# Kernel tuning notes

Measured on AMD Instinct MI355X. Metric: run time of the kernel, lower is better.

Reference implementation:

```python
import jax, jax.numpy as jnp
import numpy as np

IMG = 640.0  # square input image, strides 16/32 -> 40x40 and 20x20 grids

def _decode_level(raw, stride):
    # raw: [B, 5+C, H, W] -> [B, H*W, 5+C] with xy/wh decoded (get_output_and_grid)
    b, ch, h, w = raw.shape
    out = raw.transpose(0, 2, 3, 1).reshape(b, h * w, ch)
    yv, xv = jnp.meshgrid(jnp.arange(h), jnp.arange(w), indexing='ij')
    gx = xv.reshape(-1).astype(raw.dtype)
    gy = yv.reshape(-1).astype(raw.dtype)
    xy = (out[..., :2] + jnp.stack([gx, gy], -1)[None]) * stride
    wh = jnp.exp(out[..., 2:4]) * stride
    out = jnp.concatenate([xy, wh, out[..., 4:]], -1)
    return out, gx, gy, jnp.full((h * w,), stride, raw.dtype)

def _pairwise_iou(a, b):
    # a:[M,4], b:[A,4] in cxcywh -> [M,A] (bboxes_iou, xyxy=False)
    tl = jnp.maximum(a[:, None, :2] - a[:, None, 2:] * 0.5, b[None, :, :2] - b[None, :, 2:] * 0.5)
    br = jnp.minimum(a[:, None, :2] + a[:, None, 2:] * 0.5, b[None, :, :2] + b[None, :, 2:] * 0.5)
    inter = jnp.prod(br - tl, -1) * (tl < br).all(-1)
    area_a = a[:, 2] * a[:, 3]
    area_b = b[:, 2] * b[:, 3]
    return inter / (area_a[:, None] + area_b[None, :] - inter + 1e-16)

def _iou_loss(p, t):
    # YOLOX IOUloss (loss_type='iou'): 1 - iou^2, elementwise over [..., 4] cxcywh
    tl = jnp.maximum(p[..., :2] - p[..., 2:] * 0.5, t[..., :2] - t[..., 2:] * 0.5)
    br = jnp.minimum(p[..., :2] + p[..., 2:] * 0.5, t[..., :2] + t[..., 2:] * 0.5)
    inter = jnp.prod(br - tl, -1) * (tl < br).all(-1)
    iou = inter / (p[..., 2] * p[..., 3] + t[..., 2] * t[..., 3] - inter + 1e-16)
    return 1.0 - iou ** 2

def _bce_logits(x, t):
    # BCEWithLogitsLoss(reduction='none') = softplus(x) - x*t (stable)
    return jnp.logaddexp(0.0, x) - x * t

def _assign_one(bbox_p, cls_p, obj_p, gtb, gtc, gtv, ax, ay, st):
    # SimOTA assignment for one image (mask form of get_assignments, which is @no_grad).
    # bbox_p:[A,4] cls_p:[A,C] obj_p:[A] gtb:[M,4] px cxcywh, gtv:[M] valid mask.
    m = gtb.shape[0]
    axc = (ax + 0.5) * st
    ayc = (ay + 0.5) * st
    gl = gtb[:, 0] - 0.5 * gtb[:, 2]; gr = gtb[:, 0] + 0.5 * gtb[:, 2]
    gtp = gtb[:, 1] - 0.5 * gtb[:, 3]; gbt = gtb[:, 1] + 0.5 * gtb[:, 3]
    in_box = ((axc[None] > gl[:, None]) & (axc[None] < gr[:, None]) &
              (ayc[None] > gtp[:, None]) & (ayc[None] < gbt[:, None])) & gtv[:, None]
    r = 2.5  # center_radius
    in_ctr = ((axc[None] > gtb[:, 0:1] - r * st[None]) & (axc[None] < gtb[:, 0:1] + r * st[None]) &
              (ayc[None] > gtb[:, 1:2] - r * st[None]) & (ayc[None] < gtb[:, 1:2] + r * st[None])) & gtv[:, None]
    fg_cand = (in_box | in_ctr).any(0)          # candidate anchors (fg_mask pre-filter)
    in_both = in_box & in_ctr
    ious = _pairwise_iou(gtb, bbox_p)            # [M,A]
    p = jnp.sqrt(jax.nn.sigmoid(cls_p) * jax.nn.sigmoid(obj_p)[:, None])[None]  # [1,A,C]
    t = jax.nn.one_hot(gtc, cls_p.shape[-1], dtype=p.dtype)[:, None, :]          # [M,1,C]
    eps = 1e-12
    cls_cost = -(t * jnp.log(p + eps) + (1.0 - t) * jnp.log(1.0 - p + eps)).sum(-1)
    invalid = (~fg_cand)[None] | (~gtv)[:, None]
    cost = cls_cost - 3.0 * jnp.log(ious + 1e-8) + 1e5 * (~in_both) + 1e9 * invalid
    ious_m = jnp.where(invalid, 0.0, ious)
    topk, _ = jax.lax.top_k(ious_m, 10)
    dk = jnp.maximum(topk.sum(-1).astype(jnp.int32), 1)  # dynamic_k, clamp min=1
    dk = jnp.where(gtv, dk, 0)
    ranks = jnp.argsort(jnp.argsort(cost, axis=1), axis=1)
    matching = ranks < dk[:, None]                        # top dynamic_k lowest-cost anchors per gt
    conflict = matching.sum(0) > 1
    best_gt = jnp.argmin(cost, 0)
    matching = jnp.where(conflict[None], jnp.arange(m)[:, None] == best_gt[None], matching)
    fg = matching.any(0)
    matched = jnp.argmax(matching, 0).astype(jnp.int32)
    pred_iou = jnp.where(matching, ious, 0.0).sum(0)
    return fg, matched, pred_iou

def _forward(out_l0, out_l1, gt_boxes, gt_classes, num_gts):
    ncls = out_l0.shape[1] - 5
    decs, xs, ys, ss = [], [], [], []
    for raw, stride in ((out_l0, 16.0), (out_l1, 32.0)):
        d, gx, gy, s = _decode_level(raw, stride)
        decs.append(d); xs.append(gx); ys.append(gy); ss.append(s)
    outputs = jnp.concatenate(decs, 1)  # [B, A, 5+C]
    ax = jnp.concatenate(xs); ay = jnp.concatenate(ys); st = jnp.concatenate(ss)
    bbox_p = outputs[..., :4]; obj_p = outputs[..., 4]; cls_p = outputs[..., 5:]
    gtb = gt_boxes * IMG  # normalized -> pixels (imgs_w == imgs_h == IMG)
    gtv = jnp.arange(gt_boxes.shape[1])[None, :] < num_gts[:, None]
    sg = jax.lax.stop_gradient  # get_assignments runs under torch.no_grad
    fg, matched, pred_iou = jax.vmap(_assign_one, in_axes=(0, 0, 0, 0, 0, 0, None, None, None))(
        sg(bbox_p), sg(cls_p), sg(obj_p), sg(gtb), gt_classes, gtv, ax, ay, st)
    fgf = fg.astype(outputs.dtype)
    cls_t = jax.nn.one_hot(jnp.take_along_axis(gt_classes, matched, 1), ncls,
                           dtype=outputs.dtype) * pred_iou[..., None] * fgf[..., None]
    reg_t = jnp.take_along_axis(gtb, matched[..., None], 1)  # [B,A,4]
    num_fg = jnp.maximum(fgf.sum(), 1.0)
    loss_iou = (_iou_loss(bbox_p, reg_t) * fgf).sum() / num_fg
    loss_obj = _bce_logits(obj_p, fgf).sum() / num_fg
    loss_cls = (_bce_logits(cls_p, cls_t) * fgf[..., None]).sum() / num_fg
    total = 5.0 * loss_iou + loss_obj + loss_cls
    return (total, 5.0 * loss_iou, loss_obj, loss_cls,
            num_fg / jnp.maximum(num_gts.sum().astype(outputs.dtype), 1.0))

def setup_inputs() -> dict:
    key = jax.random.key(0)
    k1, k2, k3, k4, k5 = jax.random.split(key, 5)
    return {
        'out_l0': jax.random.normal(k1, (64, 25, 40, 40), jnp.float32),
        'out_l1': jax.random.normal(k2, (64, 25, 20, 20), jnp.float32),
        'gt_boxes': jax.random.uniform(k3, (64, 100, 4), jnp.float32, 1e-3, 1.0),
        'gt_classes': jax.random.randint(k4, (64, 100), 0, 20).astype(jnp.int32),
        'num_gts': jax.random.randint(k5, (64,), 0, 100).astype(jnp.int32),
    }

def reference(out_l0, out_l1, gt_boxes, gt_classes, num_gts):
    return _forward(out_l0, out_l1, gt_boxes, gt_classes, num_gts)
```

## Files before the change

kernel.cpp:

```cpp
#include <hip/hip_runtime.h>
#include <cfloat>
#include <climits>

#define NB 64
#define NA 2000
#define NAP 2048
#define NA0 1600
#define NC 20
#define NM 100

__device__ __forceinline__ void anchor_geom(int a, float& axc, float& ayc, float& st) {
    if (a < NA0) {
        st = 16.0f;
        int x = a % 40, y = a / 40;
        axc = ((float)x + 0.5f) * 16.0f;
        ayc = ((float)y + 0.5f) * 16.0f;
    } else {
        st = 32.0f;
        int aa = a - NA0;
        int x = aa % 20, y = aa / 20;
        axc = ((float)x + 0.5f) * 32.0f;
        ayc = ((float)y + 0.5f) * 32.0f;
    }
}

__device__ __forceinline__ float cost_pair(const float4 g, float clsc, const float4 pb,
                                           float axc, float ayc, float st, bool fc) {
    float tlx = fmaxf(g.x - 0.5f * g.z, pb.x - 0.5f * pb.z);
    float tly = fmaxf(g.y - 0.5f * g.w, pb.y - 0.5f * pb.w);
    float brx = fminf(g.x + 0.5f * g.z, pb.x + 0.5f * pb.z);
    float bry = fminf(g.y + 0.5f * g.w, pb.y + 0.5f * pb.w);
    float inter = (brx - tlx) * (bry - tly);
    bool ok = (tlx < brx) && (tly < bry);
    inter = ok ? inter : 0.0f;
    float iou = inter / ((g.z * g.w + pb.z * pb.w) - inter + 1e-16f);
    bool ib = (axc > g.x - 0.5f * g.z) && (axc < g.x + 0.5f * g.z)
           && (ayc > g.y - 0.5f * g.w) && (ayc < g.y + 0.5f * g.w);
    bool ic = (axc > g.x - 2.5f * st) && (axc < g.x + 2.5f * st)
           && (ayc > g.y - 2.5f * st) && (ayc < g.y + 2.5f * st);
    return ((clsc - 3.0f * __logf(iou + 1e-8f)) + ((ib && ic) ? 0.0f : 1e5f)) + (fc ? 0.0f : 1e9f);
}

__global__ __launch_bounds__(256) void k_decode(const float* __restrict__ l0, const float* __restrict__ l1,
                                                const float* __restrict__ gt_boxes, const int* __restrict__ num_gts,
                                                float4* __restrict__ dec, float* __restrict__ qq,
                                                unsigned long long* __restrict__ fgw, unsigned int* __restrict__ cm,
                                                unsigned int* __restrict__ counter) {
    int b = blockIdx.y;
    int a = blockIdx.x * 256 + threadIdx.x;
    int lane = threadIdx.x & 63;
    __shared__ float4 sext[NM];
    __shared__ float2 sctr[NM];
    __shared__ int sng;
    if (threadIdx.x < NM) {
        float4 g = ((const float4*)gt_boxes)[b * NM + threadIdx.x];
        g.x *= 640.0f; g.y *= 640.0f; g.z *= 640.0f; g.w *= 640.0f;
        sext[threadIdx.x] = make_float4(g.x - 0.5f * g.z, g.x + 0.5f * g.z,
                                        g.y - 0.5f * g.w, g.y + 0.5f * g.w);
        sctr[threadIdx.x] = make_float2(g.x, g.y);
    }
    if (threadIdx.x == 0) sng = num_gts[b];
    if (b == 0 && blockIdx.x == 0 && threadIdx.x == 0) *counter = 0u;
    __syncthreads();

    bool real = a < NA;
    size_t pidx = (size_t)b * NAP + a;

    if (!real) {
        dec[pidx] = make_float4(0.f, 0.f, 0.f, 0.f);
#pragma unroll
        for (int c = 0; c < NC; c++) qq[((size_t)b * NC + c) * NAP + a] = 0.0f;
        cm[pidx] = 0;
        unsigned long long mk = __ballot(0);
        if (lane == 0) fgw[(size_t)b * 32 + (a >> 6)] = mk;
        return;
    }

    float v[25];
    if (a < NA0) {
        const float* p = l0 + (size_t)b * 25 * NA0 + a;
#pragma unroll
        for (int c = 0; c < 25; c++) v[c] = p[(size_t)c * NA0];
    } else {
        const float* p = l1 + (size_t)b * 25 * 400 + (a - NA0);
#pragma unroll
        for (int c = 0; c < 25; c++) v[c] = p[(size_t)c * 400];
    }
    float axc, ayc, st;
    anchor_geom(a, axc, ayc, st);
    float gx, gy;
    if (a < NA0) { gx = (float)(a % 40); gy = (float)(a / 40); }
    else { int aa = a - NA0; gx = (float)(aa % 20); gy = (float)(aa / 20); }
    float4 pb;
    pb.x = (v[0] + gx) * st;
    pb.y = (v[1] + gy) * st;
    pb.z = expf(v[2]) * st;
    pb.w = expf(v[3]) * st;
    dec[pidx] = pb;

    float sob = 1.0f / (1.0f + __expf(-v[4]));
    float d[NC];
    float s = 0.0f;
#pragma unroll
    for (int c = 0; c < NC; c++) {
        float sc = 1.0f / (1.0f + __expf(-v[5 + c]));
        float p = sqrtf(sc * sob);
        float lp = __logf(p + 1e-12f);
        float lq = __logf(1.0f - p + 1e-12f);
        s += -lq;
        d[c] = lq - lp;
    }
#pragma unroll
    for (int c = 0; c < NC; c++)
        qq[((size_t)b * NC + c) * NAP + a] = s + d[c];

    int ng = sng;
    int f = 0;
    float rst = 2.5f * st;
    for (int m = 0; m < ng; m++) {
        float4 e = sext[m];
        float2 cc = sctr[m];
        bool ib = (axc > e.x) && (axc < e.y) && (ayc > e.z) && (ayc < e.w);
        bool ic = (axc > cc.x - rst) && (axc < cc.x + rst) && (ayc > cc.y - rst) && (ayc < cc.y + rst);
        if (ib || ic) { f = 1; break; }
    }
    unsigned long long mk = __ballot(f);
    if (lane == 0) fgw[(size_t)b * 32 + (a >> 6)] = mk;
    cm[pidx] = 0;
}

__global__ __launch_bounds__(256) void k_assign(const float* __restrict__ gt_boxes, const int* __restrict__ gt_classes,
                                                const int* __restrict__ num_gts, const float4* __restrict__ dec,
                                                const float* __restrict__ qq, const unsigned long long* __restrict__ fgw,
                                                unsigned int* __restrict__ cm) {
    int wave = threadIdx.x >> 6;
    int lane = threadIdx.x & 63;
    int row = blockIdx.x * 4 + wave;
    int b = row / NM, m = row - b * NM;
    if (m >= num_gts[b]) return;

    float4 g = ((const float4*)gt_boxes)[b * NM + m];
    g.x *= 640.0f; g.y *= 640.0f; g.z *= 640.0f; g.w *= 640.0f;
    int tc = gt_classes[b * NM + m];
    const float* qrow = qq + ((size_t)b * NC + tc) * NAP;
    size_t bNA = (size_t)b * NAP;

    float glx = g.x - 0.5f * g.z, grx = g.x + 0.5f * g.z;
    float gty = g.y - 0.5f * g.w, gby = g.y + 0.5f * g.w;
    float areag = g.z * g.w;
    float c16l = g.x - 40.0f, c16r = g.x + 40.0f, c16t = g.y - 40.0f, c16b = g.y + 40.0f;
    float c32l = g.x - 80.0f, c32r = g.x + 80.0f, c32t = g.y - 80.0f, c32b = g.y + 80.0f;

    unsigned int ik[32], ck[32];
#pragma unroll
    for (int j = 0; j < 32; j++) {
        int a = j * 64 + lane;
        float stj = (j < 25) ? 16.0f : 32.0f;
        int rel = (j < 25) ? a : (a - NA0);
        int W = (j < 25) ? 40 : 20;
        int gyv = rel / W;
        int gxv = rel - gyv * W;
        float axc = ((float)gxv + 0.5f) * stj;
        float ayc = ((float)gyv + 0.5f) * stj;
        unsigned long long fw = fgw[(size_t)b * 32 + j];
        bool fc = (fw >> lane) & 1ULL;
        float4 pb = dec[bNA + a];
        float clsc = qrow[a];
        float tlx = fmaxf(glx, pb.x - 0.5f * pb.z);
        float tly = fmaxf(gty, pb.y - 0.5f * pb.w);
        float brx = fminf(grx, pb.x + 0.5f * pb.z);
        float bry = fminf(gby, pb.y + 0.5f * pb.w);
        float inter = (brx - tlx) * (bry - tly);
        bool ok = (tlx < brx) && (tly < bry);
        inter = ok ? inter : 0.0f;
        float iou = inter / ((areag + pb.z * pb.w) - inter + 1e-16f);
        bool ib = (axc > glx) && (axc < grx) && (ayc > gty) && (ayc < gby);
        bool ic = (j < 25) ? ((axc > c16l) && (axc < c16r) && (ayc > c16t) && (ayc < c16b))
                           : ((axc > c32l) && (axc < c32r) && (ayc > c32t) && (ayc < c32b));
        float cc = ((clsc - 3.0f * __logf(iou + 1e-8f)) + ((ib && ic) ? 0.0f : 1e5f)) + (fc ? 0.0f : 1e9f);
        float im = fc ? iou : 0.0f;
        ik[j] = (__float_as_uint(im) & 0xFFFFF800u) | (unsigned)a;
        ck[j] = (__float_as_uint(cc) & 0xFFFFF800u) | (unsigned)a;
    }

    float s10 = 0.0f;
#pragma unroll 1
    for (int k = 0; k < 10; k++) {
        unsigned int t[16];
#pragma unroll
        for (int h = 0; h < 16; h++) t[h] = max(ik[2 * h], ik[2 * h + 1]);
#pragma unroll
        for (int w = 8; w >= 1; w >>= 1)
#pragma unroll
            for (int h = 0; h < w; h++) t[h] = max(t[h], t[h + w]);
        unsigned int mx = t[0];
#pragma unroll
        for (int o = 1; o < 64; o <<= 1) {
            unsigned int ov = (unsigned int)__shfl_xor((int)mx, o);
            mx = max(mx, ov);
        }
        if ((mx & 0xFFFFF800u) == 0u) break;
        s10 += __uint_as_float(mx & 0xFFFFF800u);
#pragma unroll
        for (int j = 0; j < 32; j++) ik[j] = (ik[j] == mx) ? 0u : ik[j];
    }
    int dk = (int)s10;
    if (dk < 1) dk = 1;

    unsigned int mb = 0;
#pragma unroll 1
    for (int k = 0; k < dk; k++) {
        unsigned int t[16];
#pragma unroll
        for (int h = 0; h < 16; h++) t[h] = min(ck[2 * h], ck[2 * h + 1]);
#pragma unroll
        for (int w = 8; w >= 1; w >>= 1)
#pragma unroll
            for (int h = 0; h < w; h++) t[h] = min(t[h], t[h + w]);
        unsigned int mn = t[0];
#pragma unroll
        for (int o = 1; o < 64; o <<= 1) {
            unsigned int ov = (unsigned int)__shfl_xor((int)mn, o);
            mn = min(mn, ov);
        }
#pragma unroll
        for (int j = 0; j < 32; j++) {
            bool e = (ck[j] == mn);
            mb |= e ? (1u << j) : 0u;
            ck[j] = e ? 0xFFFFFFFFu : ck[j];
        }
    }

    unsigned int inc = (1u << 20) + (unsigned)m;
#pragma unroll
    for (int j = 0; j < 32; j++) {
        if ((mb >> j) & 1u) atomicAdd(&cm[bNA + j * 64 + lane], inc);
    }
}

__global__ __launch_bounds__(256) void k_detect(const unsigned int* __restrict__ cm,
                                                unsigned int* __restrict__ list,
                                                unsigned int* __restrict__ counter) {
    int idx = blockIdx.x * 256 + threadIdx.x;
    int a = idx & (NAP - 1);
    if (a < NA && (cm[idx] >> 20) >= 2u) {
        unsigned int pos = atomicAdd(counter, 1u);
        list[pos] = (unsigned int)idx;
    }
}

__global__ __launch_bounds__(256) void k_conflict(const float* __restrict__ gt_boxes, const int* __restrict__ gt_classes,
                                                  const int* __restrict__ num_gts, const float4* __restrict__ dec,
                                                  const float* __restrict__ qq, const unsigned long long* __restrict__ fgw,
                                                  unsigned int* __restrict__ cm,
                                                  const unsigned int* __restrict__ list,
                                                  const unsigned int* __restrict__ counter) {
    int wid = (blockIdx.x * 256 + threadIdx.x) >> 6;
    int lane = threadIdx.x & 63;
    int nw = (gridDim.x * 256) >> 6;
    int cnt = (int)*counter;
    for (int i = wid; i < cnt; i += nw) {
        int idx = (int)list[i];
        int b = idx >> 11, a = idx & (NAP - 1);
        int ng = num_gts[b];
        float4 pb = dec[idx];
        float axc, ayc, st;
        anchor_geom(a, axc, ayc, st);
        bool fc = (fgw[(size_t)b * 32 + (a >> 6)] >> (a & 63)) & 1ULL;
        unsigned int best = 0xFFFFFFFFu;
#pragma unroll
        for (int half = 0; half < 2; half++) {
            int m = half * 64 + lane;
            if (m < ng) {
                float4 g = ((const float4*)gt_boxes)[b * NM + m];
                g.x *= 640.0f; g.y *= 640.0f; g.z *= 640.0f; g.w *= 640.0f;
                int tcm = gt_classes[b * NM + m];
                float clsc = qq[((size_t)b * NC + tcm) * NAP + a];
                float cc = cost_pair(g, clsc, pb, axc, ayc, st, fc);
                unsigned int key = (__float_as_uint(cc) & 0xFFFFF800u) | (unsigned)m;
                best = min(best, key);
            }
        }
#pragma unroll
        for (int o = 1; o < 64; o <<= 1) {
            unsigned int ov = (unsigned int)__shfl_xor((int)best, o);
            best = min(best, ov);
        }
        if (lane == 0) cm[idx] = (1u << 20) | (best & 0x7FFu);
    }
}

__global__ __launch_bounds__(256) void k_resolve(const float* __restrict__ l0, const float* __restrict__ l1,
                                                 const float* __restrict__ gt_boxes, const int* __restrict__ gt_classes,
                                                 const float4* __restrict__ dec,
                                                 const unsigned int* __restrict__ cm,
                                                 float* __restrict__ partials) {
    int idx = blockIdx.x * 256 + threadIdx.x;
    int b = idx / NA, a = idx - b * NA;
    size_t pidx = (size_t)b * NAP + a;

    float objv;
    if (a < NA0) objv = l0[((size_t)b * 25 + 4) * NA0 + a];
    else         objv = l1[((size_t)b * 25 + 4) * 400 + (a - NA0)];

    unsigned int word = cm[pidx];
    bool fg = (word >> 20) > 0;
    float fgf = fg ? 1.0f : 0.0f;
    float lobj = (fmaxf(objv, 0.0f) + log1pf(expf(-fabsf(objv)))) - objv * fgf;
    float liou = 0.0f, lcls = 0.0f;

    if (fg) {
        float4 pb = dec[pidx];
        int m = (int)(word & 0xFFFFFu);
        float4 g = ((const float4*)gt_boxes)[b * NM + m];
        g.x *= 640.0f; g.y *= 640.0f; g.z *= 640.0f; g.w *= 640.0f;
        float tlx = fmaxf(pb.x - 0.5f * pb.z, g.x - 0.5f * g.z);
        float tly = fmaxf(pb.y - 0.5f * pb.w, g.y - 0.5f * g.w);
        float brx = fminf(pb.x + 0.5f * pb.z, g.x + 0.5f * g.z);
        float bry = fminf(pb.y + 0.5f * pb.w, g.y + 0.5f * g.w);
        float inter = (brx - tlx) * (bry - tly);
        bool ok = (tlx < brx) && (tly < bry);
        inter = ok ? inter : 0.0f;
        float iou = inter / ((pb.z * pb.w + g.z * g.w) - inter + 1e-16f);
        liou = 1.0f - iou * iou;
        float piou = iou;
        int tcm = gt_classes[b * NM + m];
#pragma unroll
        for (int c2 = 0; c2 < NC; c2++) {
            float x;
            if (a < NA0) x = l0[((size_t)b * 25 + 5 + c2) * NA0 + a];
            else         x = l1[((size_t)b * 25 + 5 + c2) * 400 + (a - NA0)];
            float t = (c2 == tcm) ? piou : 0.0f;
            lcls += (fmaxf(x, 0.0f) + log1pf(expf(-fabsf(x)))) - x * t;
        }
    }

    __shared__ float s0[256], s1[256], s2[256], s3[256];
    int t = threadIdx.x;
    s0[t] = lobj; s1[t] = liou; s2[t] = lcls; s3[t] = fgf;
    __syncthreads();
    for (int o = 128; o > 0; o >>= 1) {
        if (t < o) { s0[t] += s0[t + o]; s1[t] += s1[t + o]; s2[t] += s2[t + o]; s3[t] += s3[t + o]; }
        __syncthreads();
    }
    if (t == 0) {
        partials[blockIdx.x * 4 + 0] = s0[0];
        partials[blockIdx.x * 4 + 1] = s1[0];
        partials[blockIdx.x * 4 + 2] = s2[0];
        partials[blockIdx.x * 4 + 3] = s3[0];
    }
}

__global__ __launch_bounds__(256) void k_final(const float* __restrict__ partials, int nblocks,
                                               const int* __restrict__ num_gts, float* __restrict__ out) {
    __shared__ float s0[256], s1[256], s2[256], s3[256];
    int t = threadIdx.x;
    float a0 = 0, a1 = 0, a2 = 0, a3 = 0;
    for (int i = t; i < nblocks; i += 256) {
        a0 += partials[i * 4 + 0];
        a1 += partials[i * 4 + 1];
        a2 += partials[i * 4 + 2];
        a3 += partials[i * 4 + 3];
    }
    s0[t] = a0; s1[t] = a1; s2[t] = a2; s3[t] = a3;
    __syncthreads();
    for (int o = 128; o > 0; o >>= 1) {
        if (t < o) { s0[t] += s0[t + o]; s1[t] += s1[t + o]; s2[t] += s2[t + o]; s3[t] += s3[t + o]; }
        __syncthreads();
    }
    if (t == 0) {
        int sg = 0;
        for (int i = 0; i < NB; i++) sg += num_gts[i];
        float num_fg = fmaxf(s3[0], 1.0f);
        float li5 = 5.0f * (s1[0] / num_fg);
        float lo = s0[0] / num_fg;
        float lcx = s2[0] / num_fg;
        out[0] = li5 + lo + lcx;
        out[1] = li5;
        out[2] = lo;
        out[3] = lcx;
        out[4] = num_fg / fmaxf((float)sg, 1.0f);
    }
}

extern "C" void kernel_launch(void* const* d_in, const int* in_sizes, int n_in,
                              void* d_out, int out_size, void* d_ws, size_t ws_size,
                              hipStream_t stream) {
    const float* l0 = (const float*)d_in[0];
    const float* l1 = (const float*)d_in[1];
    const float* gt_boxes = (const float*)d_in[2];
    const int* gt_classes = (const int*)d_in[3];
    const int* num_gts = (const int*)d_in[4];
    float* out = (float*)d_out;

    char* w = (char*)d_ws;
    float4* dec = (float4*)(w);
    float* qq   = (float*)(w + 2097152);
    unsigned long long* fgw = (unsigned long long*)(w + 12582912);
    unsigned int* cm = (unsigned int*)(w + 12599296);
    unsigned int* list = (unsigned int*)(w + 13123584);
    float* partials = (float*)(w + 13635584);
    unsigned int* counter = (unsigned int*)(w + 13643584);

    (void)n_in; (void)in_sizes; (void)out_size; (void)ws_size;

    k_decode<<<dim3(8, NB), 256, 0, stream>>>(l0, l1, gt_boxes, num_gts, dec, qq, fgw, cm, counter);
    k_assign<<<(NB * NM) / 4, 256, 0, stream>>>(gt_boxes, gt_classes, num_gts, dec, qq, fgw, cm);
    k_detect<<<(NB * NAP) / 256, 256, 0, stream>>>(cm, list, counter);
    k_conflict<<<64, 256, 0, stream>>>(gt_boxes, gt_classes, num_gts, dec, qq, fgw, cm, list, counter);
    k_resolve<<<(NB * NA) / 256, 256, 0, stream>>>(l0, l1, gt_boxes, gt_classes, dec, cm, partials);
    k_final<<<1, 256, 0, stream>>>(partials, (NB * NA) / 256, num_gts, out);
}
```

Baseline: 84.67 us.

## Compact valid GT rows and fuse conflict detection into conflict kernel via ballot

A tiny new kernel prefix-sums num_gts to build a compact list of valid (image, gt) rows, so k_assign waves map only to real rows and no longer launch and exit on padding rows. The separate detect kernel and its global atomic counter are removed. k_conflict now runs one thread per anchor, ballots which anchors have multiple matches and processes them within the wave. This swaps the atomic list build for a wide grid with mostly idle waves, and the new row-list kernel is a serial single-wave launch.

```diff
diff --git a/kernel.cpp b/kernel.cpp
--- a/kernel.cpp
+++ b/kernel.cpp
@@ -44,8 +44,7 @@
 __global__ __launch_bounds__(256) void k_decode(const float* __restrict__ l0, const float* __restrict__ l1,
                                                 const float* __restrict__ gt_boxes, const int* __restrict__ num_gts,
                                                 float4* __restrict__ dec, float* __restrict__ qq,
-                                                unsigned long long* __restrict__ fgw, unsigned int* __restrict__ cm,
-                                                unsigned int* __restrict__ counter) {
+                                                unsigned long long* __restrict__ fgw, unsigned int* __restrict__ cm) {
     int b = blockIdx.y;
     int a = blockIdx.x * 256 + threadIdx.x;
     int lane = threadIdx.x & 63;
@@ -60,7 +59,6 @@
         sctr[threadIdx.x] = make_float2(g.x, g.y);
     }
     if (threadIdx.x == 0) sng = num_gts[b];
-    if (b == 0 && blockIdx.x == 0 && threadIdx.x == 0) *counter = 0u;
     __syncthreads();
 
     bool real = a < NA;
@@ -129,15 +127,34 @@
     cm[pidx] = 0;
 }
 
+__global__ __launch_bounds__(64) void k_rows(const int* __restrict__ num_gts,
+                                             unsigned int* __restrict__ rowlist,
+                                             unsigned int* __restrict__ nrows) {
+    int lane = threadIdx.x;
+    int v = num_gts[lane];
+    int incl = v;
+#pragma unroll
+    for (int o = 1; o < 64; o <<= 1) {
+        int u = __shfl_up(incl, o, 64);
+        if (lane >= o) incl += u;
+    }
+    int excl = incl - v;
+    for (int i = 0; i < v; i++) rowlist[excl + i] = (unsigned)((lane << 7) | i);
+    if (lane == 63) nrows[0] = (unsigned)incl;
+}
+
 __global__ __launch_bounds__(256) void k_assign(const float* __restrict__ gt_boxes, const int* __restrict__ gt_classes,
-                                                const int* __restrict__ num_gts, const float4* __restrict__ dec,
+                                                const float4* __restrict__ dec,
                                                 const float* __restrict__ qq, const unsigned long long* __restrict__ fgw,
-                                                unsigned int* __restrict__ cm) {
+                                                unsigned int* __restrict__ cm,
+                                                const unsigned int* __restrict__ rowlist,
+                                                const unsigned int* __restrict__ nrows) {
     int wave = threadIdx.x >> 6;
     int lane = threadIdx.x & 63;
-    int row = blockIdx.x * 4 + wave;
-    int b = row / NM, m = row - b * NM;
-    if (m >= num_gts[b]) return;
+    int i = blockIdx.x * 4 + wave;
+    if (i >= (int)nrows[0]) return;
+    unsigned int rowcode = rowlist[i];
+    int b = rowcode >> 7, m = rowcode & 127;
 
     float4 g = ((const float4*)gt_boxes)[b * NM + m];
     g.x *= 640.0f; g.y *= 640.0f; g.z *= 640.0f; g.w *= 640.0f;
@@ -238,31 +255,23 @@
     }
 }
 
-__global__ __launch_bounds__(256) void k_detect(const unsigned int* __restrict__ cm,
-                                                unsigned int* __restrict__ list,
-                                                unsigned int* __restrict__ counter) {
-    int idx = blockIdx.x * 256 + threadIdx.x;
-    int a = idx & (NAP - 1);
-    if (a < NA && (cm[idx] >> 20) >= 2u) {
-        unsigned int pos = atomicAdd(counter, 1u);
-        list[pos] = (unsigned int)idx;
-    }
-}
-
 __global__ __launch_bounds__(256) void k_conflict(const float* __restrict__ gt_boxes, const int* __restrict__ gt_classes,
                                                   const int* __restrict__ num_gts, const float4* __restrict__ dec,
                                                   const float* __restrict__ qq, const unsigned long long* __restrict__ fgw,
-                                                  unsigned int* __restrict__ cm,
-                                                  const unsigned int* __restrict__ list,
-                                                  const unsigned int* __restrict__ counter) {
-    int wid = (blockIdx.x * 256 + threadIdx.x) >> 6;
+                                                  unsigned int* __restrict__ cm) {
+    int gtid = blockIdx.x * 256 + threadIdx.x;
     int lane = threadIdx.x & 63;
-    int nw = (gridDim.x * 256) >> 6;
-    int cnt = (int)*counter;
-    for (int i = wid; i < cnt; i += nw) {
-        int idx = (int)list[i];
-        int b = idx >> 11, a = idx & (NAP - 1);
-        int ng = num_gts[b];
+    int base = gtid & ~63;
+    unsigned int word = cm[gtid];
+    unsigned long long msk = __ballot((word >> 20) >= 2u);
+    if (msk == 0ull) return;
+    int b = base >> 11;
+    int ng = num_gts[b];
+    while (msk) {
+        int t = __ffsll((long long)msk) - 1;
+        msk &= msk - 1;
+        int idx = base + t;
+        int a = idx & (NAP - 1);
         float4 pb = dec[idx];
         float axc, ayc, st;
         anchor_geom(a, axc, ayc, st);
@@ -398,16 +407,16 @@
     float* qq   = (float*)(w + 2097152);
     unsigned long long* fgw = (unsigned long long*)(w + 12582912);
     unsigned int* cm = (unsigned int*)(w + 12599296);
-    unsigned int* list = (unsigned int*)(w + 13123584);
-    float* partials = (float*)(w + 13635584);
-    unsigned int* counter = (unsigned int*)(w + 13643584);
+    unsigned int* rowlist = (unsigned int*)(w + 13123584);
+    unsigned int* nrows = (unsigned int*)(w + 13149184);
+    float* partials = (float*)(w + 13149188);
 
     (void)n_in; (void)in_sizes; (void)out_size; (void)ws_size;
 
-    k_decode<<<dim3(8, NB), 256, 0, stream>>>(l0, l1, gt_boxes, num_gts, dec, qq, fgw, cm, counter);
-    k_assign<<<(NB * NM) / 4, 256, 0, stream>>>(gt_boxes, gt_classes, num_gts, dec, qq, fgw, cm);
-    k_detect<<<(NB * NAP) / 256, 256, 0, stream>>>(cm, list, counter);
-    k_conflict<<<64, 256, 0, stream>>>(gt_boxes, gt_classes, num_gts, dec, qq, fgw, cm, list, counter);
+    k_decode<<<dim3(8, NB), 256, 0, stream>>>(l0, l1, gt_boxes, num_gts, dec, qq, fgw, cm);
+    k_rows<<<1, 64, 0, stream>>>(num_gts, rowlist, nrows);
+    k_assign<<<(NB * NM) / 4, 256, 0, stream>>>(gt_boxes, gt_classes, dec, qq, fgw, cm, rowlist, nrows);
+    k_conflict<<<(NB * NAP) / 256, 256, 0, stream>>>(gt_boxes, gt_classes, num_gts, dec, qq, fgw, cm);
     k_resolve<<<(NB * NA) / 256, 256, 0, stream>>>(l0, l1, gt_boxes, gt_classes, dec, cm, partials);
     k_final<<<1, 256, 0, stream>>>(partials, (NB * NA) / 256, num_gts, out);
 }
```

Result: slower. 101.3 us (+19.7%).
